# Optimization experiments

Measured on AMD Instinct MI355X. Metric: run time of the kernel, lower is better.

Reference implementation:

```python
import jax, jax.numpy as jnp
import numpy as np

EPS = 1.1920928955078125e-07  # torch fp32 default eps for F.rms_norm
N_HEADS = 16
HEAD_DIM = 128


def apply_rotary_emb(x, cos, sin):
    # x: [B,S,H,D]; cos/sin: [1,S,1,D/2]
    d = x.shape[-1] // 2
    x1, x2 = x[..., :d], x[..., d:]
    return jnp.concatenate([x1 * cos + x2 * sin, -x1 * sin + x2 * cos], axis=-1)


def rms_norm(x):
    # F.rms_norm over last dim, no learned weight
    ms = jnp.mean(jnp.square(x), axis=-1, keepdims=True)
    return x * jax.lax.rsqrt(ms + EPS)


def setup_inputs() -> dict:
    key = jax.random.key(0)
    ks = jax.random.split(key, 7)
    B, S, D = 2, 2048, 2048
    half = HEAD_DIM // 2
    # rotary tables (built like standard RoPE for realism)
    inv_freq = 1.0 / (10000.0 ** (np.arange(0, half, dtype=np.float32) / half))
    t = np.arange(S, dtype=np.float32)
    freqs = np.outer(t, inv_freq)  # [S, D/2]
    cos = jnp.asarray(np.cos(freqs))[None, :, None, :]
    sin = jnp.asarray(np.sin(freqs))[None, :, None, :]
    sd = 1.0 / np.sqrt(D)
    return {
        "x": jax.random.normal(ks[0], (B, S, D), jnp.float32),
        "cos": cos,
        "sin": sin,
        "Wq": jax.random.normal(ks[1], (D, D), jnp.float32) * sd,
        "Wk": jax.random.normal(ks[2], (D, D), jnp.float32) * sd,
        "Wv": jax.random.normal(ks[3], (D, D), jnp.float32) * sd,
        "Wo": jax.random.normal(ks[4], (D, D), jnp.float32) * sd,
    }


def reference(x, cos, sin, Wq, Wk, Wv, Wo):
    B, S, D = x.shape
    H, Hd = N_HEADS, HEAD_DIM
    q = (x @ Wq.T).reshape(B, S, H, Hd)
    k = (x @ Wk.T).reshape(B, S, H, Hd)
    v = (x @ Wv.T).reshape(B, S, H, Hd)
    q = apply_rotary_emb(q, cos[:, :S], sin[:, :S])
    k = apply_rotary_emb(k, cos[:, :S], sin[:, :S])
    q = rms_norm(q) * 1.2  # [B,S,H,Hd]
    k = rms_norm(k) * 1.2
    scale = 1.0 / jnp.sqrt(jnp.asarray(Hd, x.dtype))
    # scores: [B,H,Sq,Sk]
    scores = jnp.einsum("bqhd,bkhd->bhqk", q, k) * scale
    attn = jax.nn.softmax(scores, axis=-1)
    y = jnp.einsum("bhqk,bkhd->bqhd", attn, v).reshape(B, S, D)
    return y @ Wo.T
```

## Files before the change

### kernel.cpp

```cpp
#include <hip/hip_runtime.h>
#include <hip/hip_bf16.h>
#include <math.h>

typedef __bf16 bf16;
typedef __attribute__((ext_vector_type(8))) __bf16 bf16x8;
typedef __attribute__((ext_vector_type(4))) float f32x4;
typedef __attribute__((ext_vector_type(16))) float f32x16;

#define DEV __device__ __forceinline__

DEV void gload16(const void* g, void* l) {
    __builtin_amdgcn_global_load_lds(
        (__attribute__((address_space(1))) void*)(void*)g,
        (__attribute__((address_space(3))) void*)l, 16, 0, 0);
}

DEV unsigned pk2(float a, float b) {
    union { bf16 h[2]; unsigned u; } z;
    z.h[0] = (bf16)a; z.h[1] = (bf16)b;
    return z.u;
}

DEV void plswap(unsigned& a, unsigned& b) {
    asm volatile("v_permlane32_swap_b32 %0, %1" : "+v"(a), "+v"(b));
}

DEV f32x16 mfma32(bf16x8 a, bf16x8 b, f32x16 c) {
    return __builtin_amdgcn_mfma_f32_32x32x16_bf16(a, b, c, 0, 0, 0);
}

__global__ __launch_bounds__(256) void cvt_kernel(const float* __restrict__ in,
                                                  bf16* __restrict__ out, int n8) {
    for (int i = blockIdx.x * 256 + threadIdx.x; i < n8; i += gridDim.x * 256) {
        const float4* p = (const float4*)(in + (size_t)i * 8);
        float4 a = p[0], b = p[1];
        bf16x8 o;
        o[0] = (bf16)a.x; o[1] = (bf16)a.y; o[2] = (bf16)a.z; o[3] = (bf16)a.w;
        o[4] = (bf16)b.x; o[5] = (bf16)b.y; o[6] = (bf16)b.z; o[7] = (bf16)b.w;
        *(bf16x8*)(out + (size_t)i * 8) = o;
    }
}

__global__ __launch_bounds__(256) void cvtw_kernel(const float* __restrict__ w0,
                                                   const float* __restrict__ w1,
                                                   const float* __restrict__ w2,
                                                   const float* __restrict__ w3,
                                                   bf16* __restrict__ out) {
    const float* in = (blockIdx.y == 0) ? w0 : (blockIdx.y == 1) ? w1
                      : (blockIdx.y == 2) ? w2 : w3;
    bf16* o = out + (size_t)blockIdx.y * 4194304;
    for (int i = blockIdx.x * 256 + threadIdx.x; i < 524288; i += 512 * 256) {
        const float4* p = (const float4*)(in + (size_t)i * 8);
        float4 a = p[0], b = p[1];
        bf16x8 v;
        v[0] = (bf16)a.x; v[1] = (bf16)a.y; v[2] = (bf16)a.z; v[3] = (bf16)a.w;
        v[4] = (bf16)b.x; v[5] = (bf16)b.y; v[6] = (bf16)b.z; v[7] = (bf16)b.w;
        *(bf16x8*)(o + (size_t)i * 8) = v;
    }
}

__global__ __launch_bounds__(512, 2) void gemm_qkv(const bf16* __restrict__ A,
                                                   const bf16* __restrict__ Bg,
                                                   bf16* __restrict__ outq) {
    __shared__ __align__(16) bf16 As[3][256 * 32];
    __shared__ __align__(16) bf16 Bs[3][384 * 32];
    const int tid = threadIdx.x, lane = tid & 63, wv = tid >> 6;
    const int q31 = lane & 31, h5 = lane >> 5;
    const int wm = wv >> 2, wn = wv & 3;
    const int K = 2048;

    int lin = blockIdx.x;
    int swz = (lin & 7) * 32 + (lin >> 3);
    const int tm = (swz >> 4) * 256;
    const int tn = (swz & 15) * 384;

    f32x16 acc[4][3] = {};

    auto stageA = [&](int t, int buf) {
#pragma unroll
        for (int l = 0; l < 2; ++l) {
            int chunk = l * 8 + wv;
            int row = chunk * 16 + (lane >> 2);
            int cb = ((lane & 3) * 16) ^ (((row >> 1) & 3) << 4);
            gload16((const char*)(A + (size_t)(tm + row) * K + t * 32) + cb,
                    (char*)(As[buf]) + chunk * 1024);
        }
    };
    auto stageB = [&](int t, int buf) {
#pragma unroll
        for (int l = 0; l < 3; ++l) {
            int chunk = l * 8 + wv;
            int row = chunk * 16 + (lane >> 2);
            int cb = ((lane & 3) * 16) ^ (((row >> 1) & 3) << 4);
            gload16((const char*)(Bg + (size_t)(tn + row) * K + t * 32) + cb,
                    (char*)(Bs[buf]) + chunk * 1024);
        }
    };
    auto rdA = [&](int buf, int mb, int ks) -> bf16x8 {
        int row = wm * 128 + mb * 32 + q31;
        int off = (ks * 32 + h5 * 16) ^ (((row >> 1) & 3) << 4);
        return *(const bf16x8*)((const char*)(As[buf]) + row * 64 + off);
    };
    auto rdB = [&](int buf, int nb, int ks) -> bf16x8 {
        int row = wn * 96 + nb * 32 + q31;
        int off = (ks * 32 + h5 * 16) ^ (((row >> 1) & 3) << 4);
        return *(const bf16x8*)((const char*)(Bs[buf]) + row * 64 + off);
    };

    stageA(0, 0); stageB(0, 0);
    stageA(1, 1); stageB(1, 1);
    asm volatile("s_waitcnt vmcnt(5)" ::: "memory");
    __builtin_amdgcn_s_barrier();

    int cur = 0, nxt2 = 2;
    for (int t = 0; t < 64; ++t) {
        bf16x8 af[2][2], bfr[3][2];
#pragma unroll
        for (int mb = 0; mb < 2; ++mb)
#pragma unroll
            for (int ks = 0; ks < 2; ++ks) af[mb][ks] = rdA(cur, mb, ks);
#pragma unroll
        for (int nb = 0; nb < 3; ++nb)
#pragma unroll
            for (int ks = 0; ks < 2; ++ks) bfr[nb][ks] = rdB(cur, nb, ks);
        if (t < 62) stageA(t + 2, nxt2);
        asm volatile("s_waitcnt lgkmcnt(0)" ::: "memory");
        __builtin_amdgcn_sched_barrier(0);
        __builtin_amdgcn_s_setprio(1);
#pragma unroll
        for (int mb = 0; mb < 2; ++mb)
#pragma unroll
            for (int nb = 0; nb < 3; ++nb)
#pragma unroll
                for (int ks = 0; ks < 2; ++ks)
                    acc[mb][nb] = mfma32(af[mb][ks], bfr[nb][ks], acc[mb][nb]);
        __builtin_amdgcn_s_setprio(0);
#pragma unroll
        for (int mb = 0; mb < 2; ++mb)
#pragma unroll
            for (int ks = 0; ks < 2; ++ks) af[mb][ks] = rdA(cur, 2 + mb, ks);
        if (t < 62) stageB(t + 2, nxt2);
        asm volatile("s_waitcnt lgkmcnt(0)" ::: "memory");
        __builtin_amdgcn_sched_barrier(0);
        __builtin_amdgcn_s_setprio(1);
#pragma unroll
        for (int mb = 0; mb < 2; ++mb)
#pragma unroll
            for (int nb = 0; nb < 3; ++nb)
#pragma unroll
                for (int ks = 0; ks < 2; ++ks)
                    acc[2 + mb][nb] = mfma32(af[mb][ks], bfr[nb][ks], acc[2 + mb][nb]);
        __builtin_amdgcn_s_setprio(0);
        if (t < 62)
            asm volatile("s_waitcnt vmcnt(5)" ::: "memory");
        else
            asm volatile("s_waitcnt vmcnt(0)" ::: "memory");
        __builtin_amdgcn_s_barrier();
        cur = (cur == 2) ? 0 : cur + 1;
        nxt2 = (nxt2 == 2) ? 0 : nxt2 + 1;
    }

#pragma unroll
    for (int mb = 0; mb < 4; ++mb)
#pragma unroll
        for (int nb = 0; nb < 3; ++nb) {
            int colbase = tn + wn * 96 + nb * 32;
            bf16* op = outq + (size_t)(colbase >> 11) * 8388608 +
                       (colbase & 2047) + q31;
#pragma unroll
            for (int r = 0; r < 16; ++r) {
                int row = tm + wm * 128 + mb * 32 + (r & 3) + 8 * (r >> 2) + 4 * h5;
                op[(size_t)row * 2048] = (bf16)acc[mb][nb][r];
            }
        }
}

template <bool F32OUT>
__global__ __launch_bounds__(256) void gemm_bt(const bf16* __restrict__ A,
                                               const bf16* __restrict__ B,
                                               void* __restrict__ Cout,
                                               int M, int N, int K) {
    __shared__ __align__(16) bf16 As[128 * 64];
    __shared__ __align__(16) bf16 Bs[128 * 64];
    const int tid = threadIdx.x, lane = tid & 63, wv = tid >> 6;
    int lin = blockIdx.y * 16 + blockIdx.x;
    int swz = (lin & 7) * 64 + (lin >> 3);
    const int tm = (swz >> 4) * 128, tn = (swz & 15) * 128;
    const int wr = (wv >> 1) * 64, wc = (wv & 1) * 64;

    f32x4 acc[4][4] = {};
    const int scb = (lane & 7) * 16;

    for (int k0 = 0; k0 < K; k0 += 64) {
#pragma unroll
        for (int i = 0; i < 4; ++i) {
            int chunk = wv * 4 + i;
            int row = chunk * 8 + (lane >> 3);
            int cb = scb ^ ((row & 7) << 4);
            gload16((const char*)(A + (size_t)(tm + row) * K + k0) + cb,
                    (char*)As + chunk * 1024);
            gload16((const char*)(B + (size_t)(tn + row) * K + k0) + cb,
                    (char*)Bs + chunk * 1024);
        }
        __syncthreads();
#pragma unroll
        for (int kk = 0; kk < 2; ++kk) {
            bf16x8 af[4], bfr[4];
#pragma unroll
            for (int m = 0; m < 4; ++m) {
                int row = wr + m * 16 + (lane & 15);
                int cb = (kk * 64 + ((lane >> 4) * 16)) ^ ((row & 7) << 4);
                af[m] = *(const bf16x8*)((const char*)As + row * 128 + cb);
            }
#pragma unroll
            for (int n = 0; n < 4; ++n) {
                int row = wc + n * 16 + (lane & 15);
                int cb = (kk * 64 + ((lane >> 4) * 16)) ^ ((row & 7) << 4);
                bfr[n] = *(const bf16x8*)((const char*)Bs + row * 128 + cb);
            }
#pragma unroll
            for (int m = 0; m < 4; ++m)
#pragma unroll
                for (int n = 0; n < 4; ++n)
                    acc[m][n] = __builtin_amdgcn_mfma_f32_16x16x32_bf16(
                        af[m], bfr[n], acc[m][n], 0, 0, 0);
        }
        __syncthreads();
    }
#pragma unroll
    for (int m = 0; m < 4; ++m)
#pragma unroll
        for (int n = 0; n < 4; ++n)
#pragma unroll
            for (int r = 0; r < 4; ++r) {
                int row = tm + wr + m * 16 + (lane >> 4) * 4 + r;
                int col = tn + wc + n * 16 + (lane & 15);
                if (F32OUT)
                    ((float*)Cout)[(size_t)row * N + col] = acc[m][n][r];
                else
                    ((bf16*)Cout)[(size_t)row * N + col] = (bf16)acc[m][n][r];
            }
}

__global__ __launch_bounds__(256) void rope_rms(bf16* __restrict__ q,
                                                bf16* __restrict__ k,
                                                const float* __restrict__ cosp,
                                                const float* __restrict__ sinp) {
    int gw = blockIdx.x * 4 + (threadIdx.x >> 6);
    int lane = threadIdx.x & 63;
    bf16* base = (blockIdx.y == 0) ? q : k;
    int m = gw >> 4, h = gw & 15;
    int s = m & 2047;
    bf16* p = base + (size_t)m * 2048 + h * 128;
    float x1 = (float)p[lane], x2 = (float)p[lane + 64];
    float c = cosp[s * 64 + lane], si = sinp[s * 64 + lane];
    float r1 = x1 * c + x2 * si;
    float r2 = x2 * c - x1 * si;
    float ss = r1 * r1 + r2 * r2;
#pragma unroll
    for (int msk = 1; msk < 64; msk <<= 1) ss += __shfl_xor(ss, msk);
    float sc = rsqrtf(ss * (1.0f / 128.0f) + 1.1920928955078125e-07f) * 1.2f;
    if (blockIdx.y == 0) sc *= (0.08838834764831845f * 1.4426950408889634f);
    p[lane] = (bf16)(r1 * sc);
    p[lane + 64] = (bf16)(r2 * sc);
}

__global__ __launch_bounds__(512, 2) void attn_kernel(const bf16* __restrict__ q,
                                                      const bf16* __restrict__ k,
                                                      const bf16* __restrict__ v,
                                                      bf16* __restrict__ y) {
    __shared__ __align__(16) bf16 Ks[2][64 * 128];
    __shared__ __align__(16) bf16 Vt[2][128][72];

    const int tid = threadIdx.x, lane = tid & 63, wv = tid >> 6;
    const int q31 = lane & 31, h5 = lane >> 5;

    int wgid = blockIdx.y * 8 + blockIdx.x;
    int xcd = wgid & 7, j = wgid >> 3;
    const int bh = xcd * 4 + (j >> 3);
    const int qblk = j & 7;
    const int b = bh >> 4, h = bh & 15;
    const int q0 = qblk * 256;

    const bf16* qptr = q + (size_t)(b * 2048 + q0 + wv * 32 + q31) * 2048 +
                       h * 128 + h5 * 8;
    bf16x8 qf[8];
#pragma unroll
    for (int ks = 0; ks < 8; ++ks) qf[ks] = *(const bf16x8*)(qptr + ks * 16);

    float mrun = -INFINITY, lrun = 0.f;
    f32x16 acco[4] = {};

    const int p = tid & 63, rg = tid >> 6;
    const bf16* vbase = v + (size_t)(b * 2048 + rg * 8) * 2048 + h * 128 + 2 * p;
    const bf16* kbase = k + (size_t)(b * 2048) * 2048 + h * 128;
    const int vx = ((p >> 2) & 1) << 5;

    unsigned u[8];

    auto stageK = [&](int t, int buf) {
#pragma unroll
        for (int i = 0; i < 2; ++i) {
            int chunk = wv * 2 + i;
            int row = chunk * 4 + (lane >> 4);
            int cb = ((lane & 15) * 16) ^ ((row & 7) << 4);
            gload16((const char*)(kbase + (size_t)(t * 64 + row) * 2048) + cb,
                    (char*)(Ks[buf]) + chunk * 1024);
        }
    };
    auto loadV = [&](int t) {
        const bf16* vp = vbase + (size_t)(t * 64) * 2048;
#pragma unroll
        for (int jj = 0; jj < 8; ++jj)
            u[jj] = *(const unsigned*)(vp + (size_t)jj * 2048);
    };
    auto writeV = [&](int buf) {
        union { unsigned short s[8]; bf16x8 v8; } lo, hi;
#pragma unroll
        for (int jj = 0; jj < 8; ++jj) {
            lo.s[jj] = (unsigned short)(u[jj] & 0xffff);
            hi.s[jj] = (unsigned short)(u[jj] >> 16);
        }
        char* r0 = (char*)(&Vt[buf][2 * p][0]);
        char* r1 = (char*)(&Vt[buf][2 * p + 1][0]);
        *(bf16x8*)(r0 + ((rg * 16) ^ vx)) = lo.v8;
        *(bf16x8*)(r1 + ((rg * 16) ^ vx)) = hi.v8;
    };

    stageK(0, 0);
    loadV(0);
    writeV(0);
    __syncthreads();

    const int rx = ((q31 >> 3) & 1) << 5;

    for (int t = 0; t < 32; ++t) {
        const int c = t & 1;
        if (t < 31) {
            stageK(t + 1, c ^ 1);
            loadV(t + 1);
        }

        f32x16 st[2];
        __builtin_amdgcn_s_setprio(1);
#pragma unroll
        for (int kvb = 0; kvb < 2; ++kvb) {
            f32x16 a = {};
#pragma unroll
            for (int ks = 0; ks < 8; ++ks) {
                int row = kvb * 32 + q31;
                int cb = (32 * ks + 16 * h5) ^ ((row & 7) << 4);
                const bf16x8 kf =
                    *(const bf16x8*)((const char*)(Ks[c]) + row * 256 + cb);
                a = __builtin_amdgcn_mfma_f32_32x32x16_bf16(kf, qf[ks], a, 0, 0, 0);
            }
            st[kvb] = a;
        }
        __builtin_amdgcn_s_setprio(0);

        float t8[8];
#pragma unroll
        for (int r = 0; r < 8; ++r)
            t8[r] = fmaxf(fmaxf(st[0][r], st[0][r + 8]),
                          fmaxf(st[1][r], st[1][r + 8]));
        float mx = fmaxf(fmaxf(fmaxf(t8[0], t8[1]), fmaxf(t8[2], t8[3])),
                         fmaxf(fmaxf(t8[4], t8[5]), fmaxf(t8[6], t8[7])));
        mx = fmaxf(mx, __shfl_xor(mx, 32));

        if (__any(mx - mrun > 8.0f)) {
            float mn = fmaxf(mrun, mx);
            float alpha = exp2f(mrun - mn);
            mrun = mn;
            lrun *= alpha;
#pragma unroll
            for (int r = 0; r < 16; ++r) {
                int qr = (r & 3) + 8 * (r >> 2) + 4 * h5;
                float al = __shfl(alpha, qr);
                acco[0][r] *= al; acco[1][r] *= al;
                acco[2][r] *= al; acco[3][r] *= al;
            }
        }

        unsigned w[2][8];
        float rsa = 0.f, rsb = 0.f;
#pragma unroll
        for (int kvb = 0; kvb < 2; ++kvb)
#pragma unroll
            for (int i = 0; i < 8; ++i) {
                float p0 = exp2f(st[kvb][2 * i] - mrun);
                float p1 = exp2f(st[kvb][2 * i + 1] - mrun);
                if (i & 1) rsb += p0 + p1; else rsa += p0 + p1;
                w[kvb][i] = pk2(p0, p1);
            }
        float rs = rsa + rsb;
        rs += __shfl_xor(rs, 32);
        lrun += rs;

        __builtin_amdgcn_s_setprio(1);
#pragma unroll
        for (int b2 = 0; b2 < 2; ++b2)
#pragma unroll
            for (int ksl = 0; ksl < 2; ++ksl) {
                const int ks = b2 * 2 + ksl, u0 = ksl * 4;
                unsigned f0 = w[b2][u0 + 0], f2 = w[b2][u0 + 2];
                unsigned f1 = w[b2][u0 + 1], f3 = w[b2][u0 + 3];
                plswap(f0, f2);
                plswap(f1, f3);
                union { unsigned uu[4]; bf16x8 v8; } fr;
                fr.uu[0] = f0; fr.uu[1] = f1; fr.uu[2] = f2; fr.uu[3] = f3;
#pragma unroll
                for (int dblk = 0; dblk < 4; ++dblk) {
                    const char* vrow = (const char*)(&Vt[c][dblk * 32 + q31][0]);
                    const bf16x8 vf =
                        *(const bf16x8*)(vrow + ((ks * 32 + h5 * 16) ^ rx));
                    acco[dblk] = __builtin_amdgcn_mfma_f32_32x32x16_bf16(
                        fr.v8, vf, acco[dblk], 0, 0, 0);
                }
            }
        __builtin_amdgcn_s_setprio(0);

        if (t < 31) writeV(c ^ 1);
        __syncthreads();
    }

    float linv = 1.0f / lrun;
#pragma unroll
    for (int r = 0; r < 16; ++r) {
        int qr = (r & 3) + 8 * (r >> 2) + 4 * h5;
        float il = __shfl(linv, qr);
        size_t row = (size_t)(b * 2048 + q0 + wv * 32 + qr) * 2048 + h * 128;
#pragma unroll
        for (int dblk = 0; dblk < 4; ++dblk)
            y[row + dblk * 32 + q31] = (bf16)(acco[dblk][r] * il);
    }
}

extern "C" void kernel_launch(void* const* d_in, const int* in_sizes, int n_in,
                              void* d_out, int out_size, void* d_ws, size_t ws_size,
                              hipStream_t stream) {
    const float* x = (const float*)d_in[0];
    const float* cs = (const float*)d_in[1];
    const float* sn = (const float*)d_in[2];
    const float* Wq = (const float*)d_in[3];
    const float* Wk = (const float*)d_in[4];
    const float* Wv = (const float*)d_in[5];
    const float* Wo = (const float*)d_in[6];

    char* ws = (char*)d_ws;
    bf16* xb  = (bf16*)(ws + 0);
    bf16* wqb = (bf16*)(ws + 16777216);
    bf16* wob = (bf16*)(ws + 41943040);
    bf16* qb  = (bf16*)(ws + 50331648);
    bf16* kb  = (bf16*)(ws + 67108864);
    bf16* vb  = (bf16*)(ws + 83886080);
    bf16* yb  = (bf16*)(ws + 100663296);

    cvt_kernel<<<1024, 256, 0, stream>>>(x, xb, 8388608 / 8);
    cvtw_kernel<<<dim3(512, 4), 256, 0, stream>>>(Wq, Wk, Wv, Wo, wqb);

    gemm_qkv<<<256, 512, 0, stream>>>(xb, wqb, qb);

    rope_rms<<<dim3(16384, 2), 256, 0, stream>>>(qb, kb, cs, sn);

    attn_kernel<<<dim3(8, 32), 512, 0, stream>>>(qb, kb, vb, yb);

    dim3 g(16, 32);
    gemm_bt<true><<<g, 256, 0, stream>>>(yb, wob, d_out, 4096, 2048, 2048);
}
```

Before: 285.0 us.

## Split attention KV range across two workgroups and merge partials

```diff
diff --git a/kernel.cpp b/kernel.cpp
--- a/kernel.cpp
+++ b/kernel.cpp
@@ -268,19 +268,26 @@
 __global__ __launch_bounds__(512, 2) void attn_kernel(const bf16* __restrict__ q,
                                                       const bf16* __restrict__ k,
                                                       const bf16* __restrict__ v,
-                                                      bf16* __restrict__ y) {
+                                                      bf16* __restrict__ part0,
+                                                      bf16* __restrict__ part1,
+                                                      float* __restrict__ mlbuf) {
     __shared__ __align__(16) bf16 Ks[2][64 * 128];
     __shared__ __align__(16) bf16 Vt[2][128][72];
 
     const int tid = threadIdx.x, lane = tid & 63, wv = tid >> 6;
     const int q31 = lane & 31, h5 = lane >> 5;
 
-    int wgid = blockIdx.y * 8 + blockIdx.x;
+    int wgid = blockIdx.y * 16 + blockIdx.x;
     int xcd = wgid & 7, j = wgid >> 3;
-    const int bh = xcd * 4 + (j >> 3);
-    const int qblk = j & 7;
+    const int bh = xcd * 4 + (j >> 4);
+    const int rest = j & 15;
+    const int kvs = rest >> 3;
+    const int qblk = rest & 7;
     const int b = bh >> 4, h = bh & 15;
     const int q0 = qblk * 256;
+    const int t0 = kvs * 16;
+
+    bf16* yp = kvs ? part1 : part0;
 
     const bf16* qptr = q + (size_t)(b * 2048 + q0 + wv * 32 + q31) * 2048 +
                        h * 128 + h5 * 8;
@@ -327,18 +334,18 @@
         *(bf16x8*)(r1 + ((rg * 16) ^ vx)) = hi.v8;
     };
 
-    stageK(0, 0);
-    loadV(0);
+    stageK(t0, 0);
+    loadV(t0);
     writeV(0);
     __syncthreads();
 
     const int rx = ((q31 >> 3) & 1) << 5;
 
-    for (int t = 0; t < 32; ++t) {
+    for (int t = 0; t < 16; ++t) {
         const int c = t & 1;
-        if (t < 31) {
-            stageK(t + 1, c ^ 1);
-            loadV(t + 1);
+        if (t < 15) {
+            stageK(t0 + t + 1, c ^ 1);
+            loadV(t0 + t + 1);
         }
 
         f32x16 st[2];
@@ -419,7 +426,7 @@
             }
         __builtin_amdgcn_s_setprio(0);
 
-        if (t < 31) writeV(c ^ 1);
+        if (t < 15) writeV(c ^ 1);
         __syncthreads();
     }
 
@@ -431,8 +438,39 @@
         size_t row = (size_t)(b * 2048 + q0 + wv * 32 + qr) * 2048 + h * 128;
 #pragma unroll
         for (int dblk = 0; dblk < 4; ++dblk)
-            y[row + dblk * 32 + q31] = (bf16)(acco[dblk][r] * il);
-    }
+            yp[row + dblk * 32 + q31] = (bf16)(acco[dblk][r] * il);
+    }
+    if (h5 == 0) {
+        int s = q0 + wv * 32 + q31;
+        float2 v2; v2.x = mrun; v2.y = lrun;
+        *(float2*)(mlbuf + (size_t)(((kvs * 2 + b) * 16 + h) * 2048 + s) * 2) = v2;
+    }
+}
+
+__global__ __launch_bounds__(256) void attn_combine(const bf16* __restrict__ p0,
+                                                    bf16* __restrict__ p1y,
+                                                    const float* __restrict__ ml) {
+    int idx = blockIdx.x * 256 + threadIdx.x;
+    int col8 = idx & 255;
+    int row = idx >> 8;
+    int h = col8 >> 4;
+    int b = row >> 11, s = row & 2047;
+    size_t off = (size_t)idx * 8;
+    bf16x8 o1 = *(const bf16x8*)(p0 + off);
+    bf16x8 o2 = *(const bf16x8*)(p1y + off);
+    size_t mi = (size_t)((b * 16 + h) * 2048 + s) * 2;
+    float2 a = *(const float2*)(ml + mi);
+    float2 c = *(const float2*)(ml + 131072 + mi);
+    float m = fmaxf(a.x, c.x);
+    float w1 = a.y * exp2f(a.x - m);
+    float w2 = c.y * exp2f(c.x - m);
+    float inv = 1.0f / (w1 + w2);
+    w1 *= inv; w2 *= inv;
+    bf16x8 o;
+#pragma unroll
+    for (int jj = 0; jj < 8; ++jj)
+        o[jj] = (bf16)(w1 * (float)o1[jj] + w2 * (float)o2[jj]);
+    *(bf16x8*)(p1y + off) = o;
 }
 
 extern "C" void kernel_launch(void* const* d_in, const int* in_sizes, int n_in,
@@ -454,6 +492,8 @@
     bf16* kb  = (bf16*)(ws + 67108864);
     bf16* vb  = (bf16*)(ws + 83886080);
     bf16* yb  = (bf16*)(ws + 100663296);
+    bf16* pt0 = (bf16*)(ws + 16777216);
+    float* ml = (float*)(ws + 0);
 
     cvt_kernel<<<1024, 256, 0, stream>>>(x, xb, 8388608 / 8);
     cvtw_kernel<<<dim3(512, 4), 256, 0, stream>>>(Wq, Wk, Wv, Wo, wqb);
@@ -462,7 +502,8 @@
 
     rope_rms<<<dim3(16384, 2), 256, 0, stream>>>(qb, kb, cs, sn);
 
-    attn_kernel<<<dim3(8, 32), 512, 0, stream>>>(qb, kb, vb, yb);
+    attn_kernel<<<dim3(16, 32), 512, 0, stream>>>(qb, kb, vb, pt0, yb, ml);
+    attn_combine<<<4096, 256, 0, stream>>>(pt0, yb, ml);
 
     dim3 g(16, 32);
     gemm_bt<true><<<g, 256, 0, stream>>>(yb, wob, d_out, 4096, 2048, 2048);
```

Measured after the change: 300.8 us. +5.5%, slower.
